# Optimization experiments

Hardware: AMD Instinct MI355X
Metric: run time of the kernel (lower is better)

## Reference

```python
import jax, jax.numpy as jnp
import numpy as np

B, S, E, H = 2, 2048, 1024, 16  # batch, max_seq_length, embedding_dim, num_heads
D = E // H  # head dim = 64


def setup_inputs() -> dict:
    key = jax.random.key(0)
    ks = jax.random.split(key, 7)
    scale = 0.02
    return {
        "inputs": jax.random.normal(ks[0], (B, S, E), jnp.float32),
        "embbeding_V": jax.random.normal(ks[1], (B, S, E), jnp.float32),
        "embbeding_K": jax.random.normal(ks[2], (B, S, E), jnp.float32),
        "Wq": jax.random.normal(ks[3], (E, E), jnp.float32) * scale,
        "Wk": jax.random.normal(ks[4], (E, E), jnp.float32) * scale,
        "Wv": jax.random.normal(ks[5], (E, E), jnp.float32) * scale,
        "Wo": jax.random.normal(ks[6], (E, E), jnp.float32) * scale,
    }


def reference(inputs, embbeding_V, embbeding_K, Wq, Wk, Wv, Wo):
    b = inputs.shape[0]
    # repeat last token of `inputs` to max_seq_length: [b, S, E]
    x = jnp.broadcast_to(inputs[:, -1, :][:, None, :], (b, S, E))
    # torch Linear(bias=False): y = x @ W.T ; split heads -> [b, H, S, D]
    q = (x @ Wq.T).reshape(b, S, H, D).transpose(0, 2, 1, 3)
    k = (embbeding_K @ Wk.T).reshape(b, S, H, D).transpose(0, 2, 1, 3)
    v = (embbeding_V @ Wv.T).reshape(b, S, H, D).transpose(0, 2, 1, 3)
    # UNSCALED attention (faithful to source: no 1/sqrt(d))
    s = jnp.einsum("bhqd,bhkd->bhqk", q, k)
    p = jax.nn.softmax(s, axis=-1)
    o = jnp.einsum("bhqk,bhkd->bhqd", p, v)
    # transpose(1,2) then reshape to [b, S, E]
    o = o.transpose(0, 2, 1, 3).reshape(b, S, E)
    return o @ Wo.T
```

## Files before the change

### kernel.cpp

```cpp
#include <hip/hip_runtime.h>
#include <hip/hip_bf16.h>

constexpr int B = 2, S = 2048, E = 1024, H = 16, D = 64;
constexpr int E4 = E / 4;

__device__ __forceinline__ float dot4(float4 a, float4 w) {
  return a.x * w.x + a.y * w.y + a.z * w.z + a.w * w.w;
}

__global__ void k_qvec(const float4* __restrict__ x, const float4* __restrict__ Wq,
                       float* __restrict__ q_vec) {
  int blk = blockIdx.x;
  int b = blk >> 7, n0 = (blk & 127) * 8;
  int tid = threadIdx.x;
  int nl = tid >> 5, es = tid & 31;
  const float4* xr = x + ((size_t)b * S + (S - 1)) * E4;
  const float4* wr = Wq + (size_t)(n0 + nl) * E4;
  float acc = 0.f;
#pragma unroll
  for (int j = 0; j < 8; ++j) {
    float4 a = xr[es + 32 * j];
    float4 w = wr[es + 32 * j];
    acc += dot4(a, w);
  }
#pragma unroll
  for (int o = 16; o > 0; o >>= 1) acc += __shfl_xor(acc, o, 64);
  if (es == 0) q_vec[b * E + n0 + nl] = acc;
}

__global__ void k_wkq(const float* __restrict__ q_vec, const float* __restrict__ Wk,
                      float* __restrict__ wkq, float* __restrict__ rowsum) {
  int blk = blockIdx.x;
  int eo = blk & 7;
  int bh = blk >> 3;
  int h = bh & 15;
  int tid = threadIdx.x;
  __shared__ float qh[D];
  if (tid < D) qh[tid] = q_vec[(bh >> 4) * E + h * D + tid];
  if (eo == 0 && tid == 0) rowsum[bh] = 0.f;
  __syncthreads();
  int e = eo * 128 + tid;
  const float* wp = Wk + (size_t)h * D * E + e;
  float acc = 0.f;
#pragma unroll 8
  for (int d = 0; d < D; ++d) acc += qh[d] * wp[(size_t)d * E];
  wkq[(size_t)bh * E + e] = acc;
}

__global__ __launch_bounds__(128) void k_scores_exp(const float4* __restrict__ embK,
                                                    const float4* __restrict__ wkq4,
                                                    float* __restrict__ p,
                                                    float* __restrict__ rowsum) {
  __shared__ float4 wl[H * E4];
  __shared__ float hsum[16];
  int blk = blockIdx.x;
  int b = blk >> 7, k0 = (blk & 127) * 16;
  int tid = threadIdx.x;
#pragma unroll
  for (int j = 0; j < 32; ++j)
    wl[j * 128 + tid] = wkq4[(size_t)b * (H * E4) + j * 128 + tid];
  if (tid < 16) hsum[tid] = 0.f;
  __syncthreads();
  int kp = tid >> 5, es = tid & 31;
  const float4* e0 = embK + ((size_t)b * S + k0 + kp) * E4;
  const float4* e1 = embK + ((size_t)b * S + k0 + kp + 4) * E4;
  const float4* e2 = embK + ((size_t)b * S + k0 + kp + 8) * E4;
  const float4* e3 = embK + ((size_t)b * S + k0 + kp + 12) * E4;
  float4 va[8], vb[8], vc[8], vd[8];
#pragma unroll
  for (int j = 0; j < 8; ++j) {
    va[j] = e0[es + 32 * j]; vb[j] = e1[es + 32 * j];
    vc[j] = e2[es + 32 * j]; vd[j] = e3[es + 32 * j];
  }
#pragma unroll 1
  for (int h = 0; h < H; ++h) {
    float aa = 0.f, ab = 0.f, ac = 0.f, ad = 0.f;
#pragma unroll
    for (int j = 0; j < 8; ++j) {
      float4 w = wl[h * 256 + es + 32 * j];
      aa += dot4(va[j], w); ab += dot4(vb[j], w);
      ac += dot4(vc[j], w); ad += dot4(vd[j], w);
    }
#pragma unroll
    for (int o = 16; o > 0; o >>= 1) {
      aa += __shfl_xor(aa, o, 64); ab += __shfl_xor(ab, o, 64);
      ac += __shfl_xor(ac, o, 64); ad += __shfl_xor(ad, o, 64);
    }
    if (es == 0) {
      float pa = __expf(aa), pb = __expf(ab), pc = __expf(ac), pd = __expf(ad);
      float* pr = p + ((size_t)(b * H + h)) * S + k0 + kp;
      pr[0] = pa; pr[4] = pb; pr[8] = pc; pr[12] = pd;
      atomicAdd(&hsum[h], (pa + pb) + (pc + pd));
    }
  }
  __syncthreads();
  if (tid < 16) atomicAdd(&rowsum[b * H + tid], hsum[tid]);
}

__global__ __launch_bounds__(256) void k_ctx_part(const float4* __restrict__ embV,
                                                  const float* __restrict__ p,
                                                  float4* __restrict__ part) {
  int b = blockIdx.x, eo = blockIdx.y, kz = blockIdx.z;
  int tid = threadIdx.x;
  int e4l = tid & 15, ks = tid >> 4;
  int k0 = kz * 256;
  __shared__ float pl[16 * 256];
  for (int i = tid; i < 16 * 256; i += 256) {
    int h = i >> 8, kk = i & 255;
    pl[i] = p[((size_t)(b * H + h)) * S + k0 + kk];
  }
  __syncthreads();
  const float4* pl4 = (const float4*)pl;
  int e4 = eo * 16 + e4l;
  float4 acc[H];
#pragma unroll
  for (int h = 0; h < H; ++h) acc[h] = make_float4(0.f, 0.f, 0.f, 0.f);
#pragma unroll
  for (int i4 = 0; i4 < 4; ++i4) {
    int kk = ks * 16 + i4 * 4;
    const float4* vb = embV + ((size_t)b * S + k0 + kk) * E4 + e4;
    float4 v0 = vb[0 * E4], v1 = vb[1 * E4], v2 = vb[2 * E4], v3 = vb[3 * E4];
    int kq = kk >> 2;
#pragma unroll
    for (int h = 0; h < H; ++h) {
      float4 p4 = pl4[h * 64 + kq];
      acc[h].x += p4.x * v0.x + p4.y * v1.x + p4.z * v2.x + p4.w * v3.x;
      acc[h].y += p4.x * v0.y + p4.y * v1.y + p4.z * v2.y + p4.w * v3.y;
      acc[h].z += p4.x * v0.z + p4.y * v1.z + p4.z * v2.z + p4.w * v3.z;
      acc[h].w += p4.x * v0.w + p4.y * v1.w + p4.z * v2.w + p4.w * v3.w;
    }
  }
#pragma unroll
  for (int h = 0; h < H; ++h) {
    acc[h].x += __shfl_xor(acc[h].x, 16, 64);
    acc[h].y += __shfl_xor(acc[h].y, 16, 64);
    acc[h].z += __shfl_xor(acc[h].z, 16, 64);
    acc[h].w += __shfl_xor(acc[h].w, 16, 64);
    acc[h].x += __shfl_xor(acc[h].x, 32, 64);
    acc[h].y += __shfl_xor(acc[h].y, 32, 64);
    acc[h].z += __shfl_xor(acc[h].z, 32, 64);
    acc[h].w += __shfl_xor(acc[h].w, 32, 64);
  }
  int lane = tid & 63, w = tid >> 6;
  if (lane < 16) {
    int pz = kz * 4 + w;
#pragma unroll
    for (int h = 0; h < H; ++h)
      part[((size_t)(pz * B + b) * H + h) * E4 + e4] = acc[h];
  }
}

__global__ __launch_bounds__(128) void k_reduce(const float4* __restrict__ part,
                                                float4* __restrict__ ctx4) {
  int b = blockIdx.x, h = blockIdx.y, eo = blockIdx.z;
  int tid = threadIdx.x;
  int e4l = tid & 31, psub = tid >> 5;
  int e4 = eo * 32 + e4l;
  const size_t pstride = (size_t)B * H * E4;
  const float4* pp = part + ((size_t)b * H + h) * E4 + e4 + (size_t)psub * 8 * pstride;
  float4 acc = make_float4(0.f, 0.f, 0.f, 0.f);
#pragma unroll
  for (int j = 0; j < 8; ++j) {
    float4 c = pp[j * pstride];
    acc.x += c.x; acc.y += c.y; acc.z += c.z; acc.w += c.w;
  }
  __shared__ float4 red[128];
  red[tid] = acc;
  __syncthreads();
  if (tid < 32) {
    float4 a0 = red[tid], a1 = red[tid + 32], a2 = red[tid + 64], a3 = red[tid + 96];
    float4 r = make_float4(a0.x + a1.x + a2.x + a3.x, a0.y + a1.y + a2.y + a3.y,
                           a0.z + a1.z + a2.z + a3.z, a0.w + a1.w + a2.w + a3.w);
    ctx4[((size_t)b * H + h) * E4 + e4] = r;
  }
}

__global__ void k_ovec_wave(const float* __restrict__ ctx, const float4* __restrict__ Wv4,
                            const float* __restrict__ rowsum, float* __restrict__ o_vec) {
  int gw = (blockIdx.x * blockDim.x + threadIdx.x) >> 6;
  int lane = threadIdx.x & 63;
  int b = gw >> 10, nn = gw & 1023;
  int bh = b * H + (nn >> 6);
  const float4* xr = (const float4*)(ctx + (size_t)bh * E);
  const float4* wr = Wv4 + (size_t)nn * E4;
  float acc = 0.f;
#pragma unroll
  for (int j = 0; j < 4; ++j) {
    float4 a = xr[lane + 64 * j];
    float4 w = wr[lane + 64 * j];
    acc += dot4(a, w);
  }
#pragma unroll
  for (int o = 32; o > 0; o >>= 1) acc += __shfl_xor(acc, o, 64);
  if (lane == 0) o_vec[gw] = acc / rowsum[bh];
}

__global__ void k_outvec(const float* __restrict__ o_vec, const float4* __restrict__ Wo4,
                         float* __restrict__ out_vec) {
  int gw = (blockIdx.x * blockDim.x + threadIdx.x) >> 6;
  int lane = threadIdx.x & 63;
  int b = gw >> 10, nn = gw & 1023;
  const float4* xr = (const float4*)(o_vec + (size_t)b * E);
  const float4* wr = Wo4 + (size_t)nn * E4;
  float acc = 0.f;
#pragma unroll
  for (int j = 0; j < 4; ++j) {
    float4 a = xr[lane + 64 * j];
    float4 w = wr[lane + 64 * j];
    acc += dot4(a, w);
  }
#pragma unroll
  for (int o = 32; o > 0; o >>= 1) acc += __shfl_xor(acc, o, 64);
  if (lane == 0) out_vec[gw] = acc;
}

__global__ void k_bcast(const float4* __restrict__ ov4, float4* __restrict__ out4) {
  int base = blockIdx.x * 1024 + threadIdx.x;
#pragma unroll
  for (int r = 0; r < 4; ++r) {
    int g = base + r * 256;
    out4[g] = ov4[(g >> 19) * E4 + (g & 255)];
  }
}

extern "C" void kernel_launch(void* const* d_in, const int* in_sizes, int n_in,
                              void* d_out, int out_size, void* d_ws, size_t ws_size,
                              hipStream_t stream) {
  const float* inputs = (const float*)d_in[0];
  const float* embV   = (const float*)d_in[1];
  const float* embK   = (const float*)d_in[2];
  const float* Wq     = (const float*)d_in[3];
  const float* Wk     = (const float*)d_in[4];
  const float* Wv     = (const float*)d_in[5];
  const float* Wo     = (const float*)d_in[6];

  float* ws      = (float*)d_ws;
  float* q_vec   = ws;
  float* wkq     = q_vec + B * E;
  float* p       = wkq + B * H * E;
  float* rowsum  = p + B * H * S;
  float* o_vec   = rowsum + 64;
  float* out_vec = o_vec + B * E;
  float* part    = out_vec + B * E;
  float* ctx     = part + 32 * B * H * E;

  k_qvec<<<256, 256, 0, stream>>>((const float4*)inputs, (const float4*)Wq, q_vec);
  k_wkq<<<256, 128, 0, stream>>>(q_vec, Wk, wkq, rowsum);
  k_scores_exp<<<256, 128, 0, stream>>>((const float4*)embK, (const float4*)wkq,
                                        p, rowsum);
  k_ctx_part<<<dim3(B, 16, 8), 256, 0, stream>>>((const float4*)embV, p, (float4*)part);
  k_reduce<<<dim3(B, H, 8), 128, 0, stream>>>((const float4*)part, (float4*)ctx);
  k_ovec_wave<<<512, 256, 0, stream>>>(ctx, (const float4*)Wv, rowsum, o_vec);
  k_outvec<<<512, 256, 0, stream>>>(o_vec, (const float4*)Wo, out_vec);
  k_bcast<<<1024, 256, 0, stream>>>((const float4*)out_vec, (float4*)d_out);
}
```

Before: 142.2 us.

## Fuse partial reduction into Wv projection and rebalance wkq and score kernels

The separate reduce kernel and the Wv projection kernel are merged into one kernel that sums the ctx partials into shared memory and then projects onto Wv, which removes one launch and the ctx round trip through global memory. k_ctx_part now reduces its four waves in shared memory before writing, so it emits 8 partials instead of 32. k_wkq is rewritten to use float4 row loads with a shared-memory reduction over d, and k_scores_exp uses 256-thread blocks with 8 keys per block, giving twice as many blocks. The fused kernel launches only 64 blocks, so the Wv projection runs with much less parallelism than before.

```diff
diff --git a/kernel.cpp b/kernel.cpp
--- a/kernel.cpp
+++ b/kernel.cpp
@@ -1,5 +1,4 @@
 #include <hip/hip_runtime.h>
-#include <hip/hip_bf16.h>
 
 constexpr int B = 2, S = 2048, E = 1024, H = 16, D = 64;
 constexpr int E4 = E / 4;
@@ -28,69 +27,79 @@
   if (es == 0) q_vec[b * E + n0 + nl] = acc;
 }
 
-__global__ void k_wkq(const float* __restrict__ q_vec, const float* __restrict__ Wk,
-                      float* __restrict__ wkq, float* __restrict__ rowsum) {
-  int blk = blockIdx.x;
-  int eo = blk & 7;
-  int bh = blk >> 3;
-  int h = bh & 15;
+__global__ __launch_bounds__(256) void k_wkq(const float* __restrict__ q_vec,
+                                             const float4* __restrict__ Wk4,
+                                             float4* __restrict__ wkq4,
+                                             float* __restrict__ rowsum) {
+  int bb = blockIdx.x;
+  int bh = bb >> 3, eo = bb & 7;
+  int b = bh >> 4, h = bh & 15;
   int tid = threadIdx.x;
   __shared__ float qh[D];
-  if (tid < D) qh[tid] = q_vec[(bh >> 4) * E + h * D + tid];
+  __shared__ float4 red4[256];
+  if (tid < D) qh[tid] = q_vec[b * E + h * D + tid];
   if (eo == 0 && tid == 0) rowsum[bh] = 0.f;
   __syncthreads();
-  int e = eo * 128 + tid;
-  const float* wp = Wk + (size_t)h * D * E + e;
-  float acc = 0.f;
-#pragma unroll 8
-  for (int d = 0; d < D; ++d) acc += qh[d] * wp[(size_t)d * E];
-  wkq[(size_t)bh * E + e] = acc;
-}
-
-__global__ __launch_bounds__(128) void k_scores_exp(const float4* __restrict__ embK,
+  int dq = tid >> 5, el = tid & 31;
+  int e4 = eo * 32 + el;
+  float4 acc = make_float4(0.f, 0.f, 0.f, 0.f);
+#pragma unroll
+  for (int i = 0; i < 8; ++i) {
+    int d = dq * 8 + i;
+    float qd = qh[d];
+    float4 wk = Wk4[(size_t)(h * D + d) * E4 + e4];
+    acc.x += qd * wk.x; acc.y += qd * wk.y; acc.z += qd * wk.z; acc.w += qd * wk.w;
+  }
+  red4[dq * 32 + el] = acc;
+  __syncthreads();
+  if (tid < 32) {
+    float4 r = make_float4(0.f, 0.f, 0.f, 0.f);
+#pragma unroll
+    for (int g = 0; g < 8; ++g) {
+      float4 c = red4[g * 32 + tid];
+      r.x += c.x; r.y += c.y; r.z += c.z; r.w += c.w;
+    }
+    wkq4[(size_t)bh * E4 + eo * 32 + tid] = r;
+  }
+}
+
+__global__ __launch_bounds__(256) void k_scores_exp(const float4* __restrict__ embK,
                                                     const float4* __restrict__ wkq4,
                                                     float* __restrict__ p,
                                                     float* __restrict__ rowsum) {
-  __shared__ float4 wl[H * E4];
+  __shared__ float4 wl4[H * E4];
   __shared__ float hsum[16];
-  int blk = blockIdx.x;
-  int b = blk >> 7, k0 = (blk & 127) * 16;
-  int tid = threadIdx.x;
-#pragma unroll
-  for (int j = 0; j < 32; ++j)
-    wl[j * 128 + tid] = wkq4[(size_t)b * (H * E4) + j * 128 + tid];
+  int bb = blockIdx.x;
+  int b = bb >> 8, k0 = (bb & 255) * 8;
+  int tid = threadIdx.x;
+  const float4* wsrc = wkq4 + (size_t)b * (H * E4);
+#pragma unroll
+  for (int j = 0; j < 16; ++j) wl4[j * 256 + tid] = wsrc[j * 256 + tid];
   if (tid < 16) hsum[tid] = 0.f;
   __syncthreads();
-  int kp = tid >> 5, es = tid & 31;
-  const float4* e0 = embK + ((size_t)b * S + k0 + kp) * E4;
-  const float4* e1 = embK + ((size_t)b * S + k0 + kp + 4) * E4;
-  const float4* e2 = embK + ((size_t)b * S + k0 + kp + 8) * E4;
-  const float4* e3 = embK + ((size_t)b * S + k0 + kp + 12) * E4;
-  float4 va[8], vb[8], vc[8], vd[8];
-#pragma unroll
-  for (int j = 0; j < 8; ++j) {
-    va[j] = e0[es + 32 * j]; vb[j] = e1[es + 32 * j];
-    vc[j] = e2[es + 32 * j]; vd[j] = e3[es + 32 * j];
-  }
+  int wv = tid >> 6, lane = tid & 63;
+  const float4* e0 = embK + ((size_t)b * S + k0 + wv) * E4;
+  const float4* e1 = embK + ((size_t)b * S + k0 + wv + 4) * E4;
+  float4 va[4], vb[4];
+#pragma unroll
+  for (int j = 0; j < 4; ++j) { va[j] = e0[lane + 64 * j]; vb[j] = e1[lane + 64 * j]; }
 #pragma unroll 1
   for (int h = 0; h < H; ++h) {
-    float aa = 0.f, ab = 0.f, ac = 0.f, ad = 0.f;
-#pragma unroll
-    for (int j = 0; j < 8; ++j) {
-      float4 w = wl[h * 256 + es + 32 * j];
-      aa += dot4(va[j], w); ab += dot4(vb[j], w);
-      ac += dot4(vc[j], w); ad += dot4(vd[j], w);
-    }
-#pragma unroll
-    for (int o = 16; o > 0; o >>= 1) {
-      aa += __shfl_xor(aa, o, 64); ab += __shfl_xor(ab, o, 64);
-      ac += __shfl_xor(ac, o, 64); ad += __shfl_xor(ad, o, 64);
-    }
-    if (es == 0) {
-      float pa = __expf(aa), pb = __expf(ab), pc = __expf(ac), pd = __expf(ad);
-      float* pr = p + ((size_t)(b * H + h)) * S + k0 + kp;
-      pr[0] = pa; pr[4] = pb; pr[8] = pc; pr[12] = pd;
-      atomicAdd(&hsum[h], (pa + pb) + (pc + pd));
+    float a0 = 0.f, a1 = 0.f;
+#pragma unroll
+    for (int j = 0; j < 4; ++j) {
+      float4 w = wl4[h * 256 + lane + 64 * j];
+      a0 += dot4(va[j], w); a1 += dot4(vb[j], w);
+    }
+#pragma unroll
+    for (int o = 32; o > 0; o >>= 1) {
+      a0 += __shfl_xor(a0, o, 64); a1 += __shfl_xor(a1, o, 64);
+    }
+    if (lane == 0) {
+      float p0 = __expf(a0), p1 = __expf(a1);
+      float* pr = p + ((size_t)(b * H + h)) * S + k0 + wv;
+      pr[0] = p0; pr[4] = p1;
+      atomicAdd(&hsum[h], p0 + p1);
     }
   }
   __syncthreads();
@@ -102,15 +111,15 @@
                                                   float4* __restrict__ part) {
   int b = blockIdx.x, eo = blockIdx.y, kz = blockIdx.z;
   int tid = threadIdx.x;
-  int e4l = tid & 15, ks = tid >> 4;
   int k0 = kz * 256;
   __shared__ float pl[16 * 256];
+  __shared__ float4 red4[4 * 16 * 16];
   for (int i = tid; i < 16 * 256; i += 256) {
-    int h = i >> 8, kk = i & 255;
-    pl[i] = p[((size_t)(b * H + h)) * S + k0 + kk];
+    pl[i] = p[((size_t)(b * H + (i >> 8))) * S + k0 + (i & 255)];
   }
   __syncthreads();
   const float4* pl4 = (const float4*)pl;
+  int e4l = tid & 15, ks = tid >> 4;
   int e4 = eo * 16 + e4l;
   float4 acc[H];
 #pragma unroll
@@ -118,8 +127,8 @@
 #pragma unroll
   for (int i4 = 0; i4 < 4; ++i4) {
     int kk = ks * 16 + i4 * 4;
-    const float4* vb = embV + ((size_t)b * S + k0 + kk) * E4 + e4;
-    float4 v0 = vb[0 * E4], v1 = vb[1 * E4], v2 = vb[2 * E4], v3 = vb[3 * E4];
+    const float4* vbp = embV + ((size_t)b * S + k0 + kk) * E4 + e4;
+    float4 v0 = vbp[0 * E4], v1 = vbp[1 * E4], v2 = vbp[2 * E4], v3 = vbp[3 * E4];
     int kq = kk >> 2;
 #pragma unroll
     for (int h = 0; h < H; ++h) {
@@ -130,69 +139,65 @@
       acc[h].w += p4.x * v0.w + p4.y * v1.w + p4.z * v2.w + p4.w * v3.w;
     }
   }
+  int lane = tid & 63, wv = tid >> 6;
 #pragma unroll
   for (int h = 0; h < H; ++h) {
-    acc[h].x += __shfl_xor(acc[h].x, 16, 64);
-    acc[h].y += __shfl_xor(acc[h].y, 16, 64);
-    acc[h].z += __shfl_xor(acc[h].z, 16, 64);
-    acc[h].w += __shfl_xor(acc[h].w, 16, 64);
-    acc[h].x += __shfl_xor(acc[h].x, 32, 64);
-    acc[h].y += __shfl_xor(acc[h].y, 32, 64);
-    acc[h].z += __shfl_xor(acc[h].z, 32, 64);
-    acc[h].w += __shfl_xor(acc[h].w, 32, 64);
-  }
-  int lane = tid & 63, w = tid >> 6;
+    acc[h].x += __shfl_xor(acc[h].x, 16, 64); acc[h].y += __shfl_xor(acc[h].y, 16, 64);
+    acc[h].z += __shfl_xor(acc[h].z, 16, 64); acc[h].w += __shfl_xor(acc[h].w, 16, 64);
+    acc[h].x += __shfl_xor(acc[h].x, 32, 64); acc[h].y += __shfl_xor(acc[h].y, 32, 64);
+    acc[h].z += __shfl_xor(acc[h].z, 32, 64); acc[h].w += __shfl_xor(acc[h].w, 32, 64);
+  }
   if (lane < 16) {
-    int pz = kz * 4 + w;
-#pragma unroll
-    for (int h = 0; h < H; ++h)
-      part[((size_t)(pz * B + b) * H + h) * E4 + e4] = acc[h];
-  }
-}
-
-__global__ __launch_bounds__(128) void k_reduce(const float4* __restrict__ part,
-                                                float4* __restrict__ ctx4) {
-  int b = blockIdx.x, h = blockIdx.y, eo = blockIdx.z;
-  int tid = threadIdx.x;
-  int e4l = tid & 31, psub = tid >> 5;
-  int e4 = eo * 32 + e4l;
-  const size_t pstride = (size_t)B * H * E4;
-  const float4* pp = part + ((size_t)b * H + h) * E4 + e4 + (size_t)psub * 8 * pstride;
-  float4 acc = make_float4(0.f, 0.f, 0.f, 0.f);
-#pragma unroll
-  for (int j = 0; j < 8; ++j) {
-    float4 c = pp[j * pstride];
-    acc.x += c.x; acc.y += c.y; acc.z += c.z; acc.w += c.w;
-  }
-  __shared__ float4 red[128];
-  red[tid] = acc;
-  __syncthreads();
-  if (tid < 32) {
-    float4 a0 = red[tid], a1 = red[tid + 32], a2 = red[tid + 64], a3 = red[tid + 96];
-    float4 r = make_float4(a0.x + a1.x + a2.x + a3.x, a0.y + a1.y + a2.y + a3.y,
-                           a0.z + a1.z + a2.z + a3.z, a0.w + a1.w + a2.w + a3.w);
-    ctx4[((size_t)b * H + h) * E4 + e4] = r;
-  }
-}
-
-__global__ void k_ovec_wave(const float* __restrict__ ctx, const float4* __restrict__ Wv4,
-                            const float* __restrict__ rowsum, float* __restrict__ o_vec) {
-  int gw = (blockIdx.x * blockDim.x + threadIdx.x) >> 6;
-  int lane = threadIdx.x & 63;
-  int b = gw >> 10, nn = gw & 1023;
-  int bh = b * H + (nn >> 6);
-  const float4* xr = (const float4*)(ctx + (size_t)bh * E);
-  const float4* wr = Wv4 + (size_t)nn * E4;
-  float acc = 0.f;
-#pragma unroll
-  for (int j = 0; j < 4; ++j) {
-    float4 a = xr[lane + 64 * j];
-    float4 w = wr[lane + 64 * j];
-    acc += dot4(a, w);
-  }
-#pragma unroll
-  for (int o = 32; o > 0; o >>= 1) acc += __shfl_xor(acc, o, 64);
-  if (lane == 0) o_vec[gw] = acc / rowsum[bh];
+#pragma unroll
+    for (int h = 0; h < H; ++h) red4[(wv * 16 + h) * 16 + lane] = acc[h];
+  }
+  __syncthreads();
+  {
+    int h = tid >> 4, el = tid & 15;
+    float4 r = make_float4(0.f, 0.f, 0.f, 0.f);
+#pragma unroll
+    for (int ww = 0; ww < 4; ++ww) {
+      float4 c = red4[(ww * 16 + h) * 16 + el];
+      r.x += c.x; r.y += c.y; r.z += c.z; r.w += c.w;
+    }
+    part[((size_t)(kz * B + b) * H + h) * E4 + eo * 16 + el] = r;
+  }
+}
+
+__global__ __launch_bounds__(256) void k_red_ov(const float4* __restrict__ part,
+                                                const float4* __restrict__ Wv4,
+                                                const float* __restrict__ rowsum,
+                                                float* __restrict__ o_vec) {
+  int bb = blockIdx.x;
+  int bh = bb >> 1, half = bb & 1;
+  int b = bh >> 4, h = bh & 15;
+  int tid = threadIdx.x;
+  __shared__ float4 ctxl[E4];
+  {
+    const size_t pstride = (size_t)B * H * E4;
+    const float4* pp = part + ((size_t)b * H + h) * E4 + tid;
+    float4 r = make_float4(0.f, 0.f, 0.f, 0.f);
+#pragma unroll
+    for (int pz = 0; pz < 8; ++pz) {
+      float4 c = pp[pz * pstride];
+      r.x += c.x; r.y += c.y; r.z += c.z; r.w += c.w;
+    }
+    ctxl[tid] = r;
+  }
+  __syncthreads();
+  int wv = tid >> 6, lane = tid & 63;
+  float inv_rs = rowsum[bh];
+#pragma unroll 1
+  for (int i = 0; i < 8; ++i) {
+    int n = h * D + half * 32 + wv * 8 + i;
+    const float4* wr = Wv4 + (size_t)n * E4;
+    float acc = 0.f;
+#pragma unroll
+    for (int j = 0; j < 4; ++j) acc += dot4(ctxl[lane + 64 * j], wr[lane + 64 * j]);
+#pragma unroll
+    for (int o = 32; o > 0; o >>= 1) acc += __shfl_xor(acc, o, 64);
+    if (lane == 0) o_vec[b * E + n] = acc / inv_rs;
+  }
 }
 
 __global__ void k_outvec(const float* __restrict__ o_vec, const float4* __restrict__ Wo4,
@@ -242,15 +247,13 @@
   float* o_vec   = rowsum + 64;
   float* out_vec = o_vec + B * E;
   float* part    = out_vec + B * E;
-  float* ctx     = part + 32 * B * H * E;
 
   k_qvec<<<256, 256, 0, stream>>>((const float4*)inputs, (const float4*)Wq, q_vec);
-  k_wkq<<<256, 128, 0, stream>>>(q_vec, Wk, wkq, rowsum);
-  k_scores_exp<<<256, 128, 0, stream>>>((const float4*)embK, (const float4*)wkq,
+  k_wkq<<<256, 256, 0, stream>>>(q_vec, (const float4*)Wk, (float4*)wkq, rowsum);
+  k_scores_exp<<<512, 256, 0, stream>>>((const float4*)embK, (const float4*)wkq,
                                         p, rowsum);
   k_ctx_part<<<dim3(B, 16, 8), 256, 0, stream>>>((const float4*)embV, p, (float4*)part);
-  k_reduce<<<dim3(B, H, 8), 128, 0, stream>>>((const float4*)part, (float4*)ctx);
-  k_ovec_wave<<<512, 256, 0, stream>>>(ctx, (const float4*)Wv, rowsum, o_vec);
+  k_red_ov<<<64, 256, 0, stream>>>((const float4*)part, (const float4*)Wv, rowsum, o_vec);
   k_outvec<<<512, 256, 0, stream>>>(o_vec, (const float4*)Wo, out_vec);
   k_bcast<<<1024, 256, 0, stream>>>((const float4*)out_vec, (float4*)d_out);
 }
```

Result: faster. 137.3 us (-3.5%).
